# Kernel optimization log

Measured on AMD Instinct MI355X. Metric: run time of the kernel, lower is better.

The kernel has to match this reference:

```python
import jax, jax.numpy as jnp
import numpy as np

TRAJ_NUM = 8
EVAL = 30
SGM_T = 2.0
D0 = 0.5
R = 0.3
VOX = 0.2


def setup_inputs() -> dict:
    key = jax.random.key(0)
    ks = jax.random.split(key, 6)
    G, M = 256, 4
    B = G * TRAJ_NUM
    nx, ny, nz = 400, 400, 64
    # quintic boundary matrix at t=0 and t=T; L = A^{-1}
    T = SGM_T
    A = np.array([
        [1, 0, 0, 0, 0, 0],
        [0, 1, 0, 0, 0, 0],
        [0, 0, 2, 0, 0, 0],
        [1, T, T**2, T**3, T**4, T**5],
        [0, 1, 2*T, 3*T**2, 4*T**3, 5*T**4],
        [0, 0, 2, 6*T, 12*T**2, 20*T**3]], dtype=np.float64)
    L = jnp.asarray(np.linalg.inv(A), dtype=jnp.float32)

    def state(k):
        kp, kv, ka = jax.random.split(k, 3)
        # positions inside the 80m x 80m x 12.8m map, away from borders
        p = jax.random.uniform(kp, (B, 3)) * jnp.array([70.0, 70.0, 10.0]) + jnp.array([5.0, 5.0, 1.0])
        v = jax.random.uniform(kv, (B, 3), minval=-1.0, maxval=1.0)
        a = jax.random.uniform(ka, (B, 3), minval=-0.5, maxval=0.5)
        return jnp.stack([p, v, a], axis=-1)  # (B,3,3): rows=axis, cols=[p,v,a]

    Df = state(ks[0])
    Dp = state(ks[1])
    sdf_maps = jax.random.normal(ks[2], (M, nz, ny, nx), dtype=jnp.float32) * 0.5 + 1.0  # (M,D,H,W)
    min_bounds = jnp.zeros((M, 3), jnp.float32)
    sdf_shapes = jnp.tile(jnp.array([[nx, ny, nz]], jnp.float32), (M, 1))  # (nx,ny,nz)
    map_id = jax.random.randint(ks[3], (G,), 0, M)
    return dict(Df=Df, Dp=Dp, L=L, sdf_maps=sdf_maps, min_bounds=min_bounds,
                sdf_shapes=sdf_shapes, map_id=map_id)


def _distance_cost(pos, map_id, sdf_maps, min_bounds, sdf_shapes):
    # pos: (G,N,3) world coords; replicates get_batch_sdf + grid_sample math
    mb = min_bounds[map_id]                           # (G,3)
    shp = sdf_shapes[map_id].astype(jnp.int32)        # (G,3) = (nx,ny,nz)
    mn = jnp.trunc((pos.min(1) - mb) / VOX).astype(jnp.int32)
    mx = jnp.trunc((pos.max(1) - mb) / VOX).astype(jnp.int32)
    max_spans = (mx - mn).max(0)                      # (3,) shared crop span
    c = (mn + mx) // 2
    mn = c - max_spans // 2 - 5
    mx = c + max_spans // 2 + 5
    nmn = jnp.maximum(mn, 0)
    mx = mx + (nmn - mn)
    mn = nmn
    nmx = jnp.minimum(mx, shp)
    mn = mn - (mx - nmx)
    mx = nmx
    shift = jnp.maximum(-jnp.minimum(mn, 0), 0).max(0)  # per-axis over batch
    mn = mn + shift
    local_origin = mn.astype(pos.dtype) * VOX + mb     # (G,3)
    lshape = mx - mn                                   # (G,3) int, crop size

    grid = (pos - local_origin[:, None, :]) / VOX      # local voxel coords (x,y,z)
    gp = 2.0 * grid / (lshape - 1).astype(pos.dtype)[:, None, :] - 1.0
    valid = jnp.all((gp < 0.99) & (gp > -0.99), axis=-1)  # (G,N)

    # trilinear sample, align_corners=True, zeros padding w.r.t. the crop;
    # crop voxel (i,j,k) == full-map voxel (i,j,k)+mn, so gather from the full map
    l0 = jnp.floor(grid).astype(jnp.int32)
    f = grid - l0
    Dm, Hm, Wm = sdf_maps.shape[1:]
    acc = jnp.zeros(pos.shape[:2], pos.dtype)
    for dx in (0, 1):
        for dy in (0, 1):
            for dz in (0, 1):
                il = l0 + jnp.array([dx, dy, dz], jnp.int32)       # (G,N,3) local corner
                inb = jnp.all((il >= 0) & (il < lshape[:, None, :]), axis=-1)
                ig = il + mn[:, None, :]                            # global voxel index
                gx = jnp.clip(ig[..., 0], 0, Wm - 1)
                gy = jnp.clip(ig[..., 1], 0, Hm - 1)
                gz = jnp.clip(ig[..., 2], 0, Dm - 1)
                val = sdf_maps[map_id[:, None], gz, gy, gx]         # (G,N)
                w = ((f[..., 0] if dx else 1 - f[..., 0]) *
                     (f[..., 1] if dy else 1 - f[..., 1]) *
                     (f[..., 2] if dz else 1 - f[..., 2]))
                acc = acc + jnp.where(inb, w * val, 0.0)
    dist = acc
    cost = jnp.exp(-(dist - D0) / R)
    cost = jnp.where(valid, cost, 0.0)
    return cost, dist


def reference(Df, Dp, L, sdf_maps, min_bounds, sdf_shapes, map_id):
    B = Dp.shape[0]
    # coefficients: per axis, coe = L @ [Df_row, Dp_row]
    d = jnp.concatenate([Df, Dp], axis=-1)          # (B,3,6)
    coe = jnp.einsum('jk,bik->bij', L, d)           # (B,3,6)
    dt = SGM_T / EVAL
    t = jnp.linspace(dt, SGM_T, EVAL)               # (30,)
    tp = t[:, None] ** jnp.arange(6)                # (30,6) Vandermonde
    pos = jnp.einsum('nk,bik->bni', tp, coe)        # (B,30,3)
    G = B // TRAJ_NUM
    pos_batch = pos.reshape(G, TRAJ_NUM * EVAL, 3)  # (G,N,3)
    cost, _ = _distance_cost(pos_batch, map_id, sdf_maps, min_bounds, sdf_shapes)
    cost_colli = (cost * dt).reshape(-1, EVAL).sum(-1)  # (B,)
    return cost_colli
```

## Files before the change

kernel.cpp:

```cpp
#include <hip/hip_runtime.h>
#include <hip/hip_bf16.h>
#include <math.h>

#define TRAJ 8
#define EV   30
#define NPT  (TRAJ*EV)
#define GCONST 256
#define MCONST 4
#define NXM  400
#define NYM  400
#define NZM  64

__device__ __forceinline__ float ldf(const void* p, int idx, int isbf) {
    if (isbf) return __bfloat162float(((const __hip_bfloat16*)p)[idx]);
    return ((const float*)p)[idx];
}

__device__ __forceinline__ void resolve_ms(const void*& minb,
                                           const void*& shapes) {
    if (*(const unsigned*)shapes == 0u) {
        const void* t = minb; minb = shapes; shapes = t;
    }
}

__device__ __forceinline__ int detect_bf16(const void* shapes) {
    return *(const unsigned*)shapes != 0x43C80000u;
}

__device__ __forceinline__ void build_coe(const void* Df, const void* Dp,
                                          const void* L, int g, int isbf,
                                          float* sL, float* scoe, int t) {
#pragma clang fp contract(off)
    if (t < 36) sL[t] = ldf(L, t, isbf);
    __syncthreads();
    if (t < 144) {
        int traj = t / 18, rem = t % 18, i = rem / 6, j = rem % 6;
        int b = g * TRAJ + traj;
        float dv[6];
#pragma unroll
        for (int k = 0; k < 3; ++k) {
            dv[k]     = ldf(Df, b * 9 + i * 3 + k, isbf);
            dv[3 + k] = ldf(Dp, b * 9 + i * 3 + k, isbf);
        }
        float s = 0.f;
#pragma unroll
        for (int k = 0; k < 6; ++k) s = s + sL[j * 6 + k] * dv[k];
        scoe[(traj * 3 + i) * 6 + j] = s;
    }
    __syncthreads();
}

__device__ __forceinline__ void eval_pos(const float* scoe, int traj, int e,
                                         double* p) {
    const double dt   = 2.0 / 30.0;
    const double step = (2.0 - dt) / 29.0;
    double tn = (e == EV - 1) ? 2.0 : dt + (double)e * step;
    double tk = 1.0;
    p[0] = p[1] = p[2] = 0.0;
#pragma unroll
    for (int k = 0; k < 6; ++k) {
        p[0] += tk * (double)scoe[(traj * 3 + 0) * 6 + k];
        p[1] += tk * (double)scoe[(traj * 3 + 1) * 6 + k];
        p[2] += tk * (double)scoe[(traj * 3 + 2) * 6 + k];
        tk *= tn;
    }
}

__global__ __launch_bounds__(256) void k_minmax(
    const void* Df, const void* Dp, const void* L, const void* minb_in,
    const void* shapes_in, const int* map_id, int* groupA) {
    __shared__ float  sL[36];
    __shared__ float  scoe[144];
    __shared__ double smin[3][256];
    __shared__ double smax[3][256];
    const void* minb = minb_in; const void* shapes = shapes_in;
    resolve_ms(minb, shapes);
    int g = blockIdx.x, t = threadIdx.x;
    int isbf = detect_bf16(shapes);
    build_coe(Df, Dp, L, g, isbf, sL, scoe, t);

    double p[3] = {0.0, 0.0, 0.0};
    if (t < NPT) eval_pos(scoe, t / EV, t % EV, p);
#pragma unroll
    for (int i = 0; i < 3; ++i) {
        smin[i][t] = (t < NPT) ? p[i] : 1e300;
        smax[i][t] = (t < NPT) ? p[i] : -1e300;
    }
    for (int off = 128; off; off >>= 1) {
        __syncthreads();
        if (t < off)
#pragma unroll
            for (int i = 0; i < 3; ++i) {
                smin[i][t] = fmin(smin[i][t], smin[i][t + off]);
                smax[i][t] = fmax(smax[i][t], smax[i][t + off]);
            }
    }
    __syncthreads();
    if (t == 0) {
        int mid = min(max(map_id[g], 0), MCONST - 1);
#pragma unroll
        for (int i = 0; i < 3; ++i) {
            double mb = (double)ldf(minb, mid * 3 + i, isbf);
            groupA[g * 8 + i]     = (int)trunc((smin[i][0] - mb) / 0.2);
            groupA[g * 8 + 4 + i] = (int)trunc((smax[i][0] - mb) / 0.2);
        }
    }
}

__global__ __launch_bounds__(256) void k_sample(
    const void* Df, const void* Dp, const void* L, const void* minb_in,
    const void* shapes_in, const int* map_id, const void* sdf,
    const int* groupA, float* out) {
    __shared__ float  sL[36];
    __shared__ float  scoe[144];
    __shared__ double scost[NPT];
    __shared__ int    sWin[GCONST][6];
    __shared__ int    sred[3][256];
    const void* minb = minb_in; const void* shapes = shapes_in;
    resolve_ms(minb, shapes);
    int g = blockIdx.x, t = threadIdx.x;
    int isbf = detect_bf16(shapes);

    int mn0[3], mx0[3];
#pragma unroll
    for (int i = 0; i < 3; ++i) {
        mn0[i] = groupA[t * 8 + i];
        mx0[i] = groupA[t * 8 + 4 + i];
        sred[i][t] = mx0[i] - mn0[i];
    }
    for (int off = 128; off; off >>= 1) {
        __syncthreads();
        if (t < off)
#pragma unroll
            for (int i = 0; i < 3; ++i)
                sred[i][t] = max(sred[i][t], sred[i][t + off]);
    }
    __syncthreads();
    int span[3] = {sred[0][0], sred[1][0], sred[2][0]};
    __syncthreads();

    {
        int mid_t = min(max(map_id[t], 0), MCONST - 1);
#pragma unroll
        for (int i = 0; i < 3; ++i) {
            int c   = (mn0[i] + mx0[i]) >> 1;
            int h   = span[i] >> 1;
            int mn1 = c - h - 5, mx1 = c + h + 5;
            int nmn = mn1 > 0 ? mn1 : 0;
            int mx2 = mx1 + (nmn - mn1);
            int shp = (int)ldf(shapes, mid_t * 3 + i, isbf);
            int nmx = mx2 < shp ? mx2 : shp;
            int mn3 = nmn - (mx2 - nmx);
            sWin[t][i]     = mn3;
            sWin[t][3 + i] = nmx;
            sred[i][t]     = mn3 < 0 ? -mn3 : 0;
        }
    }
    for (int off = 128; off; off >>= 1) {
        __syncthreads();
        if (t < off)
#pragma unroll
            for (int i = 0; i < 3; ++i)
                sred[i][t] = max(sred[i][t], sred[i][t + off]);
    }
    __syncthreads();
    int mnf[3], lsh[3];
#pragma unroll
    for (int i = 0; i < 3; ++i) {
        int m  = sWin[g][i] + sred[i][0];
        mnf[i] = m;
        lsh[i] = sWin[g][3 + i] - m;
    }
    __syncthreads();

    build_coe(Df, Dp, L, g, isbf, sL, scoe, t);

    int mid = min(max(map_id[g], 0), MCONST - 1);
    if (t < NPT) {
        double p[3];
        eval_pos(scoe, t / EV, t % EV, p);
        double f[3];
        int    l0[3];
        bool   valid = true;
#pragma unroll
        for (int i = 0; i < 3; ++i) {
            double mb = (double)ldf(minb, mid * 3 + i, isbf);
            double gr = (p[i] - ((double)mnf[i] * 0.2 + mb)) / 0.2;
            double gp = 2.0 * gr / (double)(lsh[i] - 1) - 1.0;
            valid = valid && (gp < 0.99) && (gp > -0.99);
            double fl = floor(gr);
            l0[i] = (int)fl;
            f[i]  = gr - fl;
        }
        const int mbase = mid * (NZM * NYM * NXM);
        int  idx8[8];
        bool inb8[8];
        double w8[8];
#pragma unroll
        for (int c = 0; c < 8; ++c) {
            int dx = c & 1, dy = (c >> 1) & 1, dz = (c >> 2) & 1;
            int ilx = l0[0] + dx, ily = l0[1] + dy, ilz = l0[2] + dz;
            inb8[c] = (ilx >= 0 && ilx < lsh[0]) && (ily >= 0 && ily < lsh[1])
                   && (ilz >= 0 && ilz < lsh[2]);
            int gx = min(max(ilx + mnf[0], 0), NXM - 1);
            int gy = min(max(ily + mnf[1], 0), NYM - 1);
            int gz = min(max(ilz + mnf[2], 0), NZM - 1);
            idx8[c] = mbase + (gz * NYM + gy) * NXM + gx;
            w8[c] = (dx ? f[0] : 1.0 - f[0]) * (dy ? f[1] : 1.0 - f[1])
                  * (dz ? f[2] : 1.0 - f[2]);
        }
        float v8[8];
#pragma unroll
        for (int c = 0; c < 8; ++c) v8[c] = ldf(sdf, idx8[c], isbf);
        double acc = 0.0;
#pragma unroll
        for (int c = 0; c < 8; ++c)
            if (inb8[c]) acc += w8[c] * (double)v8[c];

        double cost = valid ? exp(-(acc - 0.5) / 0.3) : 0.0;
        scost[t] = cost * (2.0 / 30.0);
    }
    __syncthreads();
    if (t < TRAJ) {
        double s = 0.0;
#pragma unroll
        for (int e = 0; e < EV; ++e) s += scost[t * EV + e];
        out[g * TRAJ + t] = (float)s;
    }
}

extern "C" void kernel_launch(void* const* d_in, const int* in_sizes, int n_in,
                              void* d_out, int out_size, void* d_ws,
                              size_t ws_size, hipStream_t stream) {
    int order[16];
    int n = n_in < 16 ? n_in : 16;
    for (int i = 0; i < n; ++i) order[i] = i;
    for (int i = 1; i < n; ++i) {
        int oi = order[i], j = i - 1;
        while (j >= 0 && in_sizes[order[j]] < in_sizes[oi]) {
            order[j + 1] = order[j]; --j;
        }
        order[j + 1] = oi;
    }
    const void* sdf    = d_in[order[0]];
    const void* Df     = d_in[order[1]];
    const void* Dp     = d_in[order[2]];
    const int*  map_id = (const int*)d_in[order[3]];
    const void* L      = d_in[order[4]];
    const void* minb   = d_in[order[5]];
    const void* shapes = d_in[order[6 < n ? 6 : 5]];

    int* groupA = (int*)d_ws;

    k_minmax<<<GCONST, 256, 0, stream>>>(Df, Dp, L, minb, shapes, map_id,
                                         groupA);
    k_sample<<<GCONST, 256, 0, stream>>>(Df, Dp, L, minb, shapes, map_id, sdf,
                                         groupA, (float*)d_out);
    (void)out_size; (void)ws_size;
}
```

Measured before the change: 218.8 us.

## Fuse minmax and sample kernels via cooperative grid sync

Merges the two kernels into one cooperative launch, with a grid-wide barrier between the per-group bounds pass and the sampling pass. Polynomial positions are kept in registers across the barrier, so the coefficients are not rebuilt and positions are not re-evaluated. This removes one kernel launch and the duplicated setup work. In exchange it adds a cooperative grid sync and a larger shared-memory footprint per block, which may lower occupancy.

After: 257.4 us. 1.18x slower.

```diff
diff --git a/kernel.cpp b/kernel.cpp
--- a/kernel.cpp
+++ b/kernel.cpp
@@ -1,6 +1,9 @@
 #include <hip/hip_runtime.h>
+#include <hip/hip_cooperative_groups.h>
 #include <hip/hip_bf16.h>
 #include <math.h>
+
+namespace cg = cooperative_groups;
 
 #define TRAJ 8
 #define EV   30
@@ -66,21 +69,27 @@
     }
 }
 
-__global__ __launch_bounds__(256) void k_minmax(
+__global__ __launch_bounds__(256) void SafetyLoss_30537217474583_kernel(
     const void* Df, const void* Dp, const void* L, const void* minb_in,
-    const void* shapes_in, const int* map_id, int* groupA) {
+    const void* shapes_in, const int* map_id, const void* sdf, int* groupA,
+    float* out) {
     __shared__ float  sL[36];
     __shared__ float  scoe[144];
     __shared__ double smin[3][256];
     __shared__ double smax[3][256];
+    __shared__ int    sWin[GCONST][6];
+    __shared__ int    sred[3][256];
+    __shared__ double scost[NPT];
+
     const void* minb = minb_in; const void* shapes = shapes_in;
     resolve_ms(minb, shapes);
-    int g = blockIdx.x, t = threadIdx.x;
-    int isbf = detect_bf16(shapes);
+    const int g = blockIdx.x, t = threadIdx.x;
+    const int isbf = detect_bf16(shapes);
+
     build_coe(Df, Dp, L, g, isbf, sL, scoe, t);
-
     double p[3] = {0.0, 0.0, 0.0};
     if (t < NPT) eval_pos(scoe, t / EV, t % EV, p);
+
 #pragma unroll
     for (int i = 0; i < 3; ++i) {
         smin[i][t] = (t < NPT) ? p[i] : 1e300;
@@ -97,29 +106,16 @@
     }
     __syncthreads();
     if (t == 0) {
-        int mid = min(max(map_id[g], 0), MCONST - 1);
+        int mid0 = min(max(map_id[g], 0), MCONST - 1);
 #pragma unroll
         for (int i = 0; i < 3; ++i) {
-            double mb = (double)ldf(minb, mid * 3 + i, isbf);
+            double mb = (double)ldf(minb, mid0 * 3 + i, isbf);
             groupA[g * 8 + i]     = (int)trunc((smin[i][0] - mb) / 0.2);
             groupA[g * 8 + 4 + i] = (int)trunc((smax[i][0] - mb) / 0.2);
         }
     }
-}
-
-__global__ __launch_bounds__(256) void k_sample(
-    const void* Df, const void* Dp, const void* L, const void* minb_in,
-    const void* shapes_in, const int* map_id, const void* sdf,
-    const int* groupA, float* out) {
-    __shared__ float  sL[36];
-    __shared__ float  scoe[144];
-    __shared__ double scost[NPT];
-    __shared__ int    sWin[GCONST][6];
-    __shared__ int    sred[3][256];
-    const void* minb = minb_in; const void* shapes = shapes_in;
-    resolve_ms(minb, shapes);
-    int g = blockIdx.x, t = threadIdx.x;
-    int isbf = detect_bf16(shapes);
+
+    cg::this_grid().sync();
 
     int mn0[3], mx0[3];
 #pragma unroll
@@ -171,14 +167,9 @@
         mnf[i] = m;
         lsh[i] = sWin[g][3 + i] - m;
     }
-    __syncthreads();
-
-    build_coe(Df, Dp, L, g, isbf, sL, scoe, t);
-
-    int mid = min(max(map_id[g], 0), MCONST - 1);
+
+    const int mid = min(max(map_id[g], 0), MCONST - 1);
     if (t < NPT) {
-        double p[3];
-        eval_pos(scoe, t / EV, t % EV, p);
         double f[3];
         int    l0[3];
         bool   valid = true;
@@ -193,8 +184,8 @@
             f[i]  = gr - fl;
         }
         const int mbase = mid * (NZM * NYM * NXM);
-        int  idx8[8];
-        bool inb8[8];
+        int    idx8[8];
+        bool   inb8[8];
         double w8[8];
 #pragma unroll
         for (int c = 0; c < 8; ++c) {
@@ -250,11 +241,13 @@
     const void* minb   = d_in[order[5]];
     const void* shapes = d_in[order[6 < n ? 6 : 5]];
 
-    int* groupA = (int*)d_ws;
-
-    k_minmax<<<GCONST, 256, 0, stream>>>(Df, Dp, L, minb, shapes, map_id,
-                                         groupA);
-    k_sample<<<GCONST, 256, 0, stream>>>(Df, Dp, L, minb, shapes, map_id, sdf,
-                                         groupA, (float*)d_out);
+    int*   groupA = (int*)d_ws;
+    float* outp   = (float*)d_out;
+
+    void* args[] = {(void*)&Df, (void*)&Dp, (void*)&L, (void*)&minb,
+                    (void*)&shapes, (void*)&map_id, (void*)&sdf,
+                    (void*)&groupA, (void*)&outp};
+    hipLaunchCooperativeKernel((const void*)SafetyLoss_30537217474583_kernel,
+                               dim3(GCONST), dim3(256), args, 0, stream);
     (void)out_size; (void)ws_size;
 }
```
